# Kernel tuning notes

Hardware: AMD Instinct MI355X
Metric: run time of the kernel (lower is better)

## Reference

```python
import jax, jax.numpy as jnp
import numpy as np

B, N, V, F, H, O, NCONV = 4096, 64, 100, 128, 256, 1, 4
NEG_SLOPE = 0.01  # torch nn.LeakyReLU default


def leaky(x):
    return jnp.where(x >= 0, x, NEG_SLOPE * x)


def setup_inputs() -> dict:
    key = jax.random.key(0)
    ks = jax.random.split(key, 16)
    node_mat = jax.random.normal(ks[0], (B, N, V), dtype=jnp.float32)
    a = (jax.random.uniform(ks[1], (B, N, N)) < 0.15).astype(jnp.float32)
    adj_mat = jnp.maximum(a, jnp.swapaxes(a, 1, 2))
    s = 0.05
    params = dict(
        W_init=s * jax.random.normal(ks[2], (V, F), jnp.float32),
        b_init=jnp.zeros((F,), jnp.float32),
        W_conv=s * jax.random.normal(ks[3], (NCONV, F, F), jnp.float32),
        b_conv=jnp.zeros((NCONV, F), jnp.float32),
        W_fc0=s * jax.random.normal(ks[4], (F, H), jnp.float32),
        b_fc0=jnp.zeros((H,), jnp.float32),
        W_fc1=s * jax.random.normal(ks[5], (H, H), jnp.float32),
        b_fc1=jnp.zeros((H,), jnp.float32),
        W_out=s * jax.random.normal(ks[6], (H, O), jnp.float32),
        b_out=jnp.zeros((O,), jnp.float32),
    )
    return dict(node_mat=node_mat, adj_mat=adj_mat, **params)


def reference(node_mat, adj_mat, W_init, b_init, W_conv, b_conv,
              W_fc0, b_fc0, W_fc1, b_fc1, W_out, b_out):
    # init transform + LeakyReLU
    x = leaky(node_mat @ W_init + b_init)                      # [B, N, F]
    # degree-normalized adjacency: diag(1/deg) @ A == row-scale (exact same math
    # as the original eye-expand + double bmm, without the NxN diagonal matmul)
    deg = jnp.clip(adj_mat.sum(axis=-1, keepdims=True), 1.0, None)  # [B, N, 1]
    A_norm = adj_mat / deg                                     # [B, N, N]
    for i in range(W_conv.shape[0]):
        agg = jnp.einsum('bij,bjf->bif', A_norm, x)            # neighbor mean
        x = leaky(agg @ W_conv[i] + b_conv[i])
    # mean pooling over atoms
    g = x.mean(axis=1)                                         # [B, F]
    # fc head (dropout p=0 -> identity)
    h = leaky(g @ W_fc0 + b_fc0)
    h = leaky(h @ W_fc1 + b_fc1)
    return h @ W_out + b_out                                   # [B, O]
```

## Files before the change

kernel.cpp:

```cpp
#include <hip/hip_runtime.h>

#define NATOMS 64
#define VDIM 100
#define FDIM 128
#define HDIM 256
#define NCONV 4

typedef __bf16 bf16x8 __attribute__((ext_vector_type(8)));
typedef __bf16 bf16x4 __attribute__((ext_vector_type(4)));
typedef float f32x4 __attribute__((ext_vector_type(4)));

__device__ __forceinline__ float lrelu(float x) {
  return x >= 0.0f ? x : 0.01f * x;
}

__global__ void prep_weights(const float* __restrict__ Wi,
                             const float* __restrict__ Wc,
                             __bf16* __restrict__ WtI,
                             __bf16* __restrict__ WtC) {
  int idx = blockIdx.x * 256 + threadIdx.x;
  int e = idx & 7;
  int lane = (idx >> 3) & 63;
  int ks = (idx >> 9) & 3;
  int n16 = (idx >> 11) & 7;
  int l = idx >> 14;
  int n = n16 * 16 + (lane & 15);
  int k = ks * 32 + (lane >> 4) * 8 + e;
  if (l == 0) {
    WtI[idx] = (__bf16)(k < VDIM ? Wi[k * FDIM + n] : 0.0f);
  } else {
    WtC[(l - 1) * 16384 + (idx & 16383)] =
        (__bf16)Wc[(l - 1) * FDIM * FDIM + k * FDIM + n];
  }
}

template <bool PRODUCE_FRAG>
__device__ __forceinline__ void conv_step(
    const __bf16* __restrict__ Wt, const float* __restrict__ bias,
    const __bf16* __restrict__ sRow, bf16x8 xfrag[2][2], float psum[2],
    const int w, const int lane) {
  const int lr = lane & 15;
  const int g = lane >> 4;
  const int k0 = g * 8;
  f32x4 acc[2][4];
#pragma unroll
  for (int ni = 0; ni < 2; ++ni)
#pragma unroll
    for (int mi = 0; mi < 4; ++mi) acc[ni][mi] = {0.f, 0.f, 0.f, 0.f};
#pragma unroll
  for (int ks = 0; ks < 4; ++ks) {
    bf16x8 bfrag[2], afrag[4];
#pragma unroll
    for (int ni = 0; ni < 2; ++ni)
      bfrag[ni] = *(const bf16x8*)&Wt[(((2 * w + ni) * 4 + ks) * 64 + lane) * 8];
#pragma unroll
    for (int mi = 0; mi < 4; ++mi) {
      int m = mi * 16 + lr;
      afrag[mi] = *(const bf16x8*)&sRow[m * 128 + ((ks * 32 + k0) ^ ((m & 7) << 3))];
    }
#pragma unroll
    for (int ni = 0; ni < 2; ++ni)
#pragma unroll
      for (int mi = 0; mi < 4; ++mi)
        acc[ni][mi] = __builtin_amdgcn_mfma_f32_16x16x32_bf16(
            afrag[mi], bfrag[ni], acc[ni][mi], 0, 0, 0);
  }
#pragma unroll
  for (int ni = 0; ni < 2; ++ni) {
    float bv = bias[(2 * w + ni) * 16 + lr];
    if constexpr (PRODUCE_FRAG) {
      uint2 d[4];
#pragma unroll
      for (int mi = 0; mi < 4; ++mi) {
        bf16x4 o;
#pragma unroll
        for (int j = 0; j < 4; ++j) o[j] = (__bf16)lrelu(acc[ni][mi][j] + bv);
        d[mi] = __builtin_bit_cast(uint2, o);
      }
#pragma unroll
      for (int ksp = 0; ksp < 2; ++ksp) {
        unsigned r[4];
#pragma unroll
        for (int q = 0; q < 4; ++q) {
          int src = (2 * (g & 1) + (q >> 1)) * 16 + lr;
          unsigned lo = (q & 1) ? d[2 * ksp].y : d[2 * ksp].x;
          unsigned hi = (q & 1) ? d[2 * ksp + 1].y : d[2 * ksp + 1].x;
          unsigned va = (unsigned)__shfl((int)lo, src);
          unsigned vb = (unsigned)__shfl((int)hi, src);
          r[q] = (g >> 1) ? vb : va;
        }
        xfrag[ni][ksp] =
            __builtin_bit_cast(bf16x8, make_uint4(r[0], r[1], r[2], r[3]));
      }
    } else {
      float s = 0.f;
#pragma unroll
      for (int mi = 0; mi < 4; ++mi)
#pragma unroll
        for (int j = 0; j < 4; ++j) s += lrelu(acc[ni][mi][j] + bv);
      psum[ni] = s;
    }
  }
}

__device__ __forceinline__ void agg_step(const __bf16* __restrict__ sAdj,
                                         const bf16x8 xfrag[2][2],
                                         __bf16* __restrict__ sRow,
                                         const float rdgv[4], const int w,
                                         const int lane) {
  const int lr = lane & 15;
  const int g = lane >> 4;
  const int k0 = g * 8;
  f32x4 acc[2][4];
#pragma unroll
  for (int mi = 0; mi < 2; ++mi)
#pragma unroll
    for (int ni = 0; ni < 4; ++ni) acc[mi][ni] = {0.f, 0.f, 0.f, 0.f};
#pragma unroll
  for (int ks = 0; ks < 2; ++ks) {
    bf16x8 bfrag[4];
#pragma unroll
    for (int ni = 0; ni < 4; ++ni) {
      int n = ni * 16 + lr;
      bfrag[ni] = *(const bf16x8*)&sAdj[n * 64 + ((ks * 32 + k0) ^ ((n & 7) << 3))];
    }
#pragma unroll
    for (int mi = 0; mi < 2; ++mi)
#pragma unroll
      for (int ni = 0; ni < 4; ++ni)
        acc[mi][ni] = __builtin_amdgcn_mfma_f32_16x16x32_bf16(
            xfrag[mi][ks], bfrag[ni], acc[mi][ni], 0, 0, 0);
  }
#pragma unroll
  for (int ni = 0; ni < 4; ++ni) {
    float rv = rdgv[ni];
    int a = ni * 16 + lr;
#pragma unroll
    for (int mi = 0; mi < 2; ++mi) {
      int f0r = (2 * w + mi) * 16 + g * 4;
      bf16x4 o;
#pragma unroll
      for (int j = 0; j < 4; ++j) o[j] = (__bf16)(acc[mi][ni][j] * rv);
      *(bf16x4*)&sRow[a * 128 + (f0r ^ ((a & 7) << 3))] = o;
    }
  }
}

__launch_bounds__(256, 8)
__global__ void gcn_mfma(const float* __restrict__ node,
                         const float* __restrict__ adj,
                         const __bf16* __restrict__ WtI,
                         const __bf16* __restrict__ WtC,
                         const float* __restrict__ b_init,
                         const float* __restrict__ b_conv,
                         float* __restrict__ g_out) {
  __shared__ __align__(16) __bf16 sRow[NATOMS * FDIM];
  __shared__ __align__(16) __bf16 sAdj[NATOMS * NATOMS];
  __shared__ float sRdg[NATOMS];

  const int b = blockIdx.x;
  const int t = threadIdx.x;
  const int lane = t & 63;
  const int w = t >> 6;

  {
    const float* adjB = adj + (size_t)b * NATOMS * NATOMS;
#pragma unroll
    for (int half = 0; half < 2; ++half) {
      int n = (t >> 3) + half * 32;
      int gi = t & 7;
      float4 a0 = *(const float4*)&adjB[n * 64 + gi * 8];
      float4 a1 = *(const float4*)&adjB[n * 64 + gi * 8 + 4];
      bf16x8 v;
      v[0] = (__bf16)a0.x; v[1] = (__bf16)a0.y; v[2] = (__bf16)a0.z; v[3] = (__bf16)a0.w;
      v[4] = (__bf16)a1.x; v[5] = (__bf16)a1.y; v[6] = (__bf16)a1.z; v[7] = (__bf16)a1.w;
      *(bf16x8*)&sAdj[n * 64 + ((gi * 8) ^ ((n & 7) << 3))] = v;
      float p = a0.x + a0.y + a0.z + a0.w + a1.x + a1.y + a1.z + a1.w;
      p += __shfl_xor(p, 1); p += __shfl_xor(p, 2); p += __shfl_xor(p, 4);
      if (gi == 0) sRdg[n] = 1.0f / fmaxf(p, 1.0f);
    }
  }
  {
    const float* nodeB = node + (size_t)b * NATOMS * VDIM;
#pragma unroll
    for (int u0 = 0; u0 < 4; ++u0) {
      int u = t + 256 * u0;
      int n = u >> 4, gi = u & 15, kk = gi * 8;
      bf16x8 v;
      if (kk + 8 <= VDIM) {
        float4 a0 = *(const float4*)&nodeB[n * VDIM + kk];
        float4 a1 = *(const float4*)&nodeB[n * VDIM + kk + 4];
        v[0] = (__bf16)a0.x; v[1] = (__bf16)a0.y; v[2] = (__bf16)a0.z; v[3] = (__bf16)a0.w;
        v[4] = (__bf16)a1.x; v[5] = (__bf16)a1.y; v[6] = (__bf16)a1.z; v[7] = (__bf16)a1.w;
      } else {
#pragma unroll
        for (int i = 0; i < 8; ++i)
          v[i] = (__bf16)((kk + i < VDIM) ? nodeB[n * VDIM + kk + i] : 0.0f);
      }
      *(bf16x8*)&sRow[n * 128 + (kk ^ ((n & 7) << 3))] = v;
    }
  }
  __syncthreads();

  float rdgv[4];
#pragma unroll
  for (int ni = 0; ni < 4; ++ni) rdgv[ni] = sRdg[ni * 16 + (lane & 15)];

  bf16x8 xfrag[2][2];
  float psum[2];

  conv_step<true>(WtI, b_init, sRow, xfrag, psum, w, lane);
  __syncthreads();

#pragma unroll
  for (int l = 0; l < NCONV; ++l) {
    agg_step(sAdj, xfrag, sRow, rdgv, w, lane);
    __syncthreads();
    if (l < NCONV - 1) {
      conv_step<true>(WtC + l * 16384, b_conv + l * FDIM, sRow, xfrag, psum, w, lane);
      __syncthreads();
    } else {
      conv_step<false>(WtC + l * 16384, b_conv + l * FDIM, sRow, xfrag, psum, w, lane);
    }
  }

#pragma unroll
  for (int ni = 0; ni < 2; ++ni) {
    float s = psum[ni];
    s += __shfl_xor(s, 16);
    s += __shfl_xor(s, 32);
    if (lane < 16)
      g_out[(size_t)b * FDIM + (2 * w + ni) * 16 + lane] = s * (1.0f / 64.0f);
  }
}

__launch_bounds__(256, 2)
__global__ void head_fc(const float* __restrict__ g,
                        const float* __restrict__ W_fc0, const float* __restrict__ b_fc0,
                        const float* __restrict__ W_fc1, const float* __restrict__ b_fc1,
                        const float* __restrict__ W_out, const float* __restrict__ b_out,
                        float* __restrict__ out) {
  __shared__ __align__(16) float sG[16 * FDIM];
  __shared__ float sH[16 * (HDIM + 1)];
  __shared__ float sRed[4 * 16];

  const int t = threadIdx.x;
  const int lane = t & 63;
  const int w = t >> 6;
  const int r0 = blockIdx.x * 16;

  {
    const float4* gs = (const float4*)(g + (size_t)r0 * FDIM);
    float4* gd = (float4*)sG;
#pragma unroll
    for (int u = 0; u < 2; ++u) gd[t + 256 * u] = gs[t + 256 * u];
  }
  __syncthreads();

  float acc[16];
  {
    float bv = b_fc0[t];
#pragma unroll
    for (int r = 0; r < 16; ++r) acc[r] = bv;
    for (int k = 0; k < FDIM; ++k) {
      float wv = W_fc0[k * HDIM + t];
#pragma unroll
      for (int r = 0; r < 16; ++r) acc[r] += sG[r * FDIM + k] * wv;
    }
#pragma unroll
    for (int r = 0; r < 16; ++r) sH[r * (HDIM + 1) + t] = lrelu(acc[r]);
  }
  __syncthreads();

  {
    float bv = b_fc1[t];
#pragma unroll
    for (int r = 0; r < 16; ++r) acc[r] = bv;
    for (int k = 0; k < HDIM; ++k) {
      float wv = W_fc1[k * HDIM + t];
#pragma unroll
      for (int r = 0; r < 16; ++r) acc[r] += sH[r * (HDIM + 1) + k] * wv;
    }
    float wo = W_out[t];
#pragma unroll
    for (int r = 0; r < 16; ++r) acc[r] = lrelu(acc[r]) * wo;
  }
#pragma unroll
  for (int r = 0; r < 16; ++r) {
    float v = acc[r];
    v += __shfl_down(v, 32); v += __shfl_down(v, 16); v += __shfl_down(v, 8);
    v += __shfl_down(v, 4);  v += __shfl_down(v, 2);  v += __shfl_down(v, 1);
    if (lane == 0) sRed[w * 16 + r] = v;
  }
  __syncthreads();
  if (t < 16)
    out[r0 + t] = sRed[t] + sRed[16 + t] + sRed[32 + t] + sRed[48 + t] + b_out[0];
}

extern "C" void kernel_launch(void* const* d_in, const int* in_sizes, int n_in,
                              void* d_out, int out_size, void* d_ws, size_t ws_size,
                              hipStream_t stream) {
  (void)in_sizes; (void)n_in; (void)ws_size; (void)out_size;
  const float* node   = (const float*)d_in[0];
  const float* adj    = (const float*)d_in[1];
  const float* W_init = (const float*)d_in[2];
  const float* b_init = (const float*)d_in[3];
  const float* W_conv = (const float*)d_in[4];
  const float* b_conv = (const float*)d_in[5];
  const float* W_fc0  = (const float*)d_in[6];
  const float* b_fc0  = (const float*)d_in[7];
  const float* W_fc1  = (const float*)d_in[8];
  const float* b_fc1  = (const float*)d_in[9];
  const float* W_out  = (const float*)d_in[10];
  const float* b_out  = (const float*)d_in[11];
  float* out = (float*)d_out;

  __bf16* WtI = (__bf16*)d_ws;
  __bf16* WtC = WtI + 16384;
  float* g = (float*)((char*)d_ws + 160 * 1024);

  prep_weights<<<320, 256, 0, stream>>>(W_init, W_conv, WtI, WtC);
  gcn_mfma<<<4096, 256, 0, stream>>>(node, adj, WtI, WtC, b_init, b_conv, g);
  head_fc<<<256, 256, 0, stream>>>(g, W_fc0, b_fc0, W_fc1, b_fc1, W_out, b_out, out);
}
```

Measured before the change: 144.8 us.

## Make GCN kernel persistent and prefetch next molecule's node features into LDS

The per-molecule kernel becomes a persistent kernel of 768 blocks, each looping over molecules with a grid stride. While the current molecule's conv and aggregation steps run, the next molecule's node features are fetched in slices into a new fp32 LDS staging buffer. This is meant to hide global-load latency behind MFMA work. The staging buffer roughly doubles per-block LDS use, which lowers resident blocks per CU. 4096 molecules do not split evenly over 768 blocks, and the adjacency load is still not prefetched.

```diff
diff --git a/kernel.cpp b/kernel.cpp
--- a/kernel.cpp
+++ b/kernel.cpp
@@ -5,6 +5,8 @@
 #define FDIM 128
 #define HDIM 256
 #define NCONV 4
+#define NBLOCKS 768
+#define NMOLS 4096
 
 typedef __bf16 bf16x8 __attribute__((ext_vector_type(8)));
 typedef __bf16 bf16x4 __attribute__((ext_vector_type(4)));
@@ -157,80 +159,120 @@
   __shared__ __align__(16) __bf16 sRow[NATOMS * FDIM];
   __shared__ __align__(16) __bf16 sAdj[NATOMS * NATOMS];
   __shared__ float sRdg[NATOMS];
-
-  const int b = blockIdx.x;
+  __shared__ __align__(16) float sStageN[NATOMS * VDIM];
+
   const int t = threadIdx.x;
   const int lane = t & 63;
   const int w = t >> 6;
-
-  {
-    const float* adjB = adj + (size_t)b * NATOMS * NATOMS;
-#pragma unroll
-    for (int half = 0; half < 2; ++half) {
-      int n = (t >> 3) + half * 32;
-      int gi = t & 7;
-      float4 a0 = *(const float4*)&adjB[n * 64 + gi * 8];
-      float4 a1 = *(const float4*)&adjB[n * 64 + gi * 8 + 4];
-      bf16x8 v;
-      v[0] = (__bf16)a0.x; v[1] = (__bf16)a0.y; v[2] = (__bf16)a0.z; v[3] = (__bf16)a0.w;
-      v[4] = (__bf16)a1.x; v[5] = (__bf16)a1.y; v[6] = (__bf16)a1.z; v[7] = (__bf16)a1.w;
-      *(bf16x8*)&sAdj[n * 64 + ((gi * 8) ^ ((n & 7) << 3))] = v;
-      float p = a0.x + a0.y + a0.z + a0.w + a1.x + a1.y + a1.z + a1.w;
-      p += __shfl_xor(p, 1); p += __shfl_xor(p, 2); p += __shfl_xor(p, 4);
-      if (gi == 0) sRdg[n] = 1.0f / fmaxf(p, 1.0f);
-    }
-  }
-  {
-    const float* nodeB = node + (size_t)b * NATOMS * VDIM;
+  const int lr = lane & 15;
+
+  auto slice_issue = [&](int mol, int s, float4& pf) {
+    int i = s * 256 + t;
+    if (i < 1600) pf = ((const float4*)(node + (size_t)mol * NATOMS * VDIM))[i];
+  };
+  auto slice_write = [&](int s, float4& pf) {
+    int i = s * 256 + t;
+    if (i < 1600) *(float4*)&sStageN[i * 4] = pf;
+  };
+  auto convert_node = [&]() {
 #pragma unroll
     for (int u0 = 0; u0 < 4; ++u0) {
       int u = t + 256 * u0;
       int n = u >> 4, gi = u & 15, kk = gi * 8;
       bf16x8 v;
       if (kk + 8 <= VDIM) {
-        float4 a0 = *(const float4*)&nodeB[n * VDIM + kk];
-        float4 a1 = *(const float4*)&nodeB[n * VDIM + kk + 4];
+        float4 a0 = *(const float4*)&sStageN[n * VDIM + kk];
+        float4 a1 = *(const float4*)&sStageN[n * VDIM + kk + 4];
         v[0] = (__bf16)a0.x; v[1] = (__bf16)a0.y; v[2] = (__bf16)a0.z; v[3] = (__bf16)a0.w;
         v[4] = (__bf16)a1.x; v[5] = (__bf16)a1.y; v[6] = (__bf16)a1.z; v[7] = (__bf16)a1.w;
+      } else if (kk < VDIM) {
+        float4 a0 = *(const float4*)&sStageN[n * VDIM + kk];
+        v[0] = (__bf16)a0.x; v[1] = (__bf16)a0.y; v[2] = (__bf16)a0.z; v[3] = (__bf16)a0.w;
+        v[4] = (__bf16)0.f; v[5] = (__bf16)0.f; v[6] = (__bf16)0.f; v[7] = (__bf16)0.f;
       } else {
 #pragma unroll
-        for (int i = 0; i < 8; ++i)
-          v[i] = (__bf16)((kk + i < VDIM) ? nodeB[n * VDIM + kk + i] : 0.0f);
+        for (int i = 0; i < 8; ++i) v[i] = (__bf16)0.f;
       }
       *(bf16x8*)&sRow[n * 128 + (kk ^ ((n & 7) << 3))] = v;
     }
+  };
+
+  {
+    const float4* src = (const float4*)(node + (size_t)blockIdx.x * NATOMS * VDIM);
+#pragma unroll
+    for (int s = 0; s < 7; ++s) {
+      int i = s * 256 + t;
+      if (i < 1600) *(float4*)&sStageN[i * 4] = src[i];
+    }
   }
   __syncthreads();
 
-  float rdgv[4];
-#pragma unroll
-  for (int ni = 0; ni < 4; ++ni) rdgv[ni] = sRdg[ni * 16 + (lane & 15)];
-
-  bf16x8 xfrag[2][2];
-  float psum[2];
-
-  conv_step<true>(WtI, b_init, sRow, xfrag, psum, w, lane);
-  __syncthreads();
-
-#pragma unroll
-  for (int l = 0; l < NCONV; ++l) {
-    agg_step(sAdj, xfrag, sRow, rdgv, w, lane);
+  float4 pf;
+
+  for (int m = blockIdx.x; m < NMOLS; m += NBLOCKS) {
+    const int mn = m + NBLOCKS;
+    const bool pre = mn < NMOLS;
+
+    convert_node();
+    {
+      const float* adjB = adj + (size_t)m * NATOMS * NATOMS;
+#pragma unroll
+      for (int half = 0; half < 2; ++half) {
+        int n = (t >> 3) + half * 32;
+        int gi = t & 7;
+        float4 a0 = *(const float4*)&adjB[n * 64 + gi * 8];
+        float4 a1 = *(const float4*)&adjB[n * 64 + gi * 8 + 4];
+        bf16x8 v;
+        v[0] = (__bf16)a0.x; v[1] = (__bf16)a0.y; v[2] = (__bf16)a0.z; v[3] = (__bf16)a0.w;
+        v[4] = (__bf16)a1.x; v[5] = (__bf16)a1.y; v[6] = (__bf16)a1.z; v[7] = (__bf16)a1.w;
+        *(bf16x8*)&sAdj[n * 64 + ((gi * 8) ^ ((n & 7) << 3))] = v;
+        float p = a0.x + a0.y + a0.z + a0.w + a1.x + a1.y + a1.z + a1.w;
+        p += __shfl_xor(p, 1); p += __shfl_xor(p, 2); p += __shfl_xor(p, 4);
+        if (gi == 0) sRdg[n] = 1.0f / fmaxf(p, 1.0f);
+      }
+    }
     __syncthreads();
-    if (l < NCONV - 1) {
-      conv_step<true>(WtC + l * 16384, b_conv + l * FDIM, sRow, xfrag, psum, w, lane);
+
+    float rdgv[4];
+#pragma unroll
+    for (int ni = 0; ni < 4; ++ni) rdgv[ni] = sRdg[ni * 16 + lr];
+
+    bf16x8 xfrag[2][2];
+    float psum[2];
+
+    conv_step<true>(WtI, b_init, sRow, xfrag, psum, w, lane);
+    if (pre) slice_issue(mn, 0, pf);
+    __syncthreads();
+
+#pragma unroll
+    for (int l = 0; l < NCONV; ++l) {
+      agg_step(sAdj, xfrag, sRow, rdgv, w, lane);
+      if (pre) {
+        slice_write(2 * l, pf);
+        if (2 * l + 1 < 7) slice_issue(mn, 2 * l + 1, pf);
+      }
       __syncthreads();
-    } else {
-      conv_step<false>(WtC + l * 16384, b_conv + l * FDIM, sRow, xfrag, psum, w, lane);
-    }
-  }
-
-#pragma unroll
-  for (int ni = 0; ni < 2; ++ni) {
-    float s = psum[ni];
-    s += __shfl_xor(s, 16);
-    s += __shfl_xor(s, 32);
-    if (lane < 16)
-      g_out[(size_t)b * FDIM + (2 * w + ni) * 16 + lane] = s * (1.0f / 64.0f);
+      if (l < NCONV - 1) {
+        conv_step<true>(WtC + l * 16384, b_conv + l * FDIM, sRow, xfrag, psum, w, lane);
+        if (pre) {
+          slice_write(2 * l + 1, pf);
+          slice_issue(mn, 2 * l + 2, pf);
+        }
+        __syncthreads();
+      } else {
+        conv_step<false>(WtC + l * 16384, b_conv + l * FDIM, sRow, xfrag, psum, w, lane);
+      }
+    }
+
+#pragma unroll
+    for (int ni = 0; ni < 2; ++ni) {
+      float s = psum[ni];
+      s += __shfl_xor(s, 16);
+      s += __shfl_xor(s, 32);
+      if (lane < 16)
+        g_out[(size_t)m * FDIM + (2 * w + ni) * 16 + lane] = s * (1.0f / 64.0f);
+    }
+    __syncthreads();
   }
 }
 
@@ -320,6 +362,6 @@
   float* g = (float*)((char*)d_ws + 160 * 1024);
 
   prep_weights<<<320, 256, 0, stream>>>(W_init, W_conv, WtI, WtC);
-  gcn_mfma<<<4096, 256, 0, stream>>>(node, adj, WtI, WtC, b_init, b_conv, g);
+  gcn_mfma<<<NBLOCKS, 256, 0, stream>>>(node, adj, WtI, WtC, b_init, b_conv, g);
   head_fc<<<256, 256, 0, stream>>>(g, W_fc0, b_fc0, W_fc1, b_fc1, W_out, b_out, out);
 }
```

New measurement: 191.0 us. 32.0% more time.
